# Kernel tuning notes

Hardware: AMD Instinct MI355X
Metric: run time of the kernel (lower is better)

The kernel has to match this reference:

```python
import jax, jax.numpy as jnp
import numpy as np

C = 256
HEADS = 8
HEAD_DIM = C // HEADS
SCALE = HEAD_DIM ** -0.5
POOL = 2
LN_EPS = 1e-5


def setup_inputs() -> dict:
    key = jax.random.key(0)
    ks = jax.random.split(key, 10)
    B, H, W = 8, 64, 64
    std = 0.02
    return {
        "x": jax.random.normal(ks[0], (B, C, H, W), jnp.float32),
        "Wq": jax.random.normal(ks[1], (HEADS, C), jnp.float32) * std,
        "Wk": jax.random.normal(ks[2], (HEADS, C), jnp.float32) * std,
        "Wv": jax.random.normal(ks[3], (C, C), jnp.float32) * std,
        "Wsr": jax.random.normal(ks[4], (C, C), jnp.float32) * (2.0 / C) ** 0.5,
        "bsr": jnp.zeros((C,), jnp.float32),
        "gamma": jnp.ones((C,), jnp.float32),
        "beta": jnp.zeros((C,), jnp.float32),
        "Wp": jax.random.normal(ks[5], (C, C), jnp.float32) * std,
        "bp": jnp.zeros((C,), jnp.float32),
    }


def reference(x, Wq, Wk, Wv, Wsr, bsr, gamma, beta, Wp, bp):
    B, Cc, H, W = x.shape
    N = H * W
    # tokens [B, N, C]
    tok = x.reshape(B, Cc, N).transpose(0, 2, 1)
    # q: Linear(C -> heads), per-head scalar query  [B, heads, N]
    q = jnp.einsum("bnc,hc->bhn", tok, Wq)
    # spatial reduction: avgpool(pool_ratio) then 1x1 conv
    xp = x.reshape(B, Cc, H // POOL, POOL, W // POOL, POOL).mean(axis=(3, 5))
    xs = jnp.einsum("bchw,oc->bohw", xp, Wsr) + bsr[None, :, None, None]
    M = (H // POOL) * (W // POOL)
    x_ = xs.reshape(B, Cc, M).transpose(0, 2, 1)  # [B, M, C]
    # LayerNorm + GELU (exact erf, torch default)
    mu = x_.mean(-1, keepdims=True)
    var = ((x_ - mu) ** 2).mean(-1, keepdims=True)
    x_ = (x_ - mu) * jax.lax.rsqrt(var + LN_EPS) * gamma + beta
    x_ = jax.nn.gelu(x_, approximate=False)
    # k: per-head scalar key [B, heads, M]; v: [B, heads, M, head_dim]
    k = jnp.einsum("bmc,hc->bhm", x_, Wk)
    v = jnp.einsum("bmc,oc->bmo", x_, Wv).reshape(B, M, HEADS, HEAD_DIM).transpose(0, 2, 1, 3)
    # rank-1 attention scores [B, heads, N, M]
    attn = jax.nn.softmax(q[:, :, :, None] * k[:, :, None, :] * SCALE, axis=-1)
    out = jnp.einsum("bhnm,bhmd->bhnd", attn, v)  # [B, heads, N, head_dim]
    out = out.transpose(0, 2, 1, 3).reshape(B, N, Cc)
    out = out @ Wp.T + bp
    return out.transpose(0, 2, 1).reshape(B, Cc, H, W)
```

## Files before the change

kernel.cpp:

```cpp
#include <hip/hip_runtime.h>
#include <math.h>


#define NH 8
#define NJ 8
#define NT (NH * NJ)
#define SCALE 0.17677669529663687f

__device__ __constant__ float INVFACT[NJ] = {
    1.0f, 1.0f, 0.5f, 1.6666666666666666e-01f, 4.1666666666666664e-02f,
    8.3333333333333332e-03f, 1.3888888888888889e-03f, 1.9841269841269841e-04f};

__global__ void k0_q_prep(const float* __restrict__ x, const float* __restrict__ Wq,
                          const float* __restrict__ Wsr, const float* __restrict__ Wv,
                          float* __restrict__ q01, float* __restrict__ WsrT,
                          float* __restrict__ WvT) {
    __shared__ float wq[NH * 128];
    const int tid = threadIdx.x;
    const int blk = blockIdx.x;
    if (blk < 256) {
        const int b = blk >> 5, half = (blk >> 4) & 1, nt = blk & 15;
#pragma unroll
        for (int r = 0; r < 4; ++r) {
            int idx = r * 256 + tid;
            int h = idx >> 7, cc = idx & 127;
            wq[idx] = Wq[h * 256 + half * 128 + cc];
        }
        __syncthreads();
        const int n = nt * 256 + tid;
        const float* xb = x + (((size_t)b << 8) + half * 128) * 4096 + n;
        float acc[NH] = {};
#pragma unroll 8
        for (int c = 0; c < 128; ++c) {
            float xv = xb[(size_t)c << 12];
#pragma unroll
            for (int h = 0; h < NH; ++h) acc[h] += xv * wq[h * 128 + c];
        }
#pragma unroll
        for (int h = 0; h < NH; ++h)
            q01[((size_t)(half * 64 + b * 8 + h) << 12) + n] = acc[h];
    } else {
        const float* W = (blk < 288) ? Wsr : Wv;
        float* WT = (blk < 288) ? WsrT : WvT;
        const int c0 = (blk & 31) * 8;
#pragma unroll
        for (int r = 0; r < 2; ++r) {
            int fidx = r * 256 + tid;
            int c = c0 + (fidx >> 6), o4 = (fidx & 63) * 4;
            float4 t;
            t.x = W[(size_t)(o4 + 0) * 256 + c];
            t.y = W[(size_t)(o4 + 1) * 256 + c];
            t.z = W[(size_t)(o4 + 2) * 256 + c];
            t.w = W[(size_t)(o4 + 3) * 256 + c];
            *(float4*)&WT[(size_t)c * 256 + o4] = t;
        }
    }
}

__global__ void ka_mega(const float* __restrict__ x, const float* __restrict__ WsrT,
                        const float* __restrict__ bsr, const float* __restrict__ WvT,
                        const float* __restrict__ gamma, const float* __restrict__ beta,
                        const float* __restrict__ Wk,
                        float* __restrict__ v, float* __restrict__ kout) {
    __shared__ float smem[20352];
    float* a_pool = smem;
    float* wpan   = smem + 1152;
    float* g_lds  = smem + 9472;
    float4* wkv   = (float4*)(smem + 17792);
    float4* glv   = (float4*)(smem + 19840);
    float4* blv   = (float4*)(smem + 20096);

    const int tid = threadIdx.x;
    const int blk = blockIdx.x;
    const int b = blk >> 5, mt = blk & 31;
    const int m0 = mt * 32;
    const int i2 = mt;

    const int ccs = tid >> 3, jg = tid & 7;
    const int mg = tid & 7, og = tid >> 3;

    const float4* Wk4 = (const float4*)Wk;
    wkv[tid] = Wk4[tid];
    wkv[256 + tid] = Wk4[256 + tid];
    if (tid < 64) {
        glv[tid] = ((const float4*)gamma)[tid];
        blv[tid] = ((const float4*)beta)[tid];
    }

    float acc[4][8] = {};
    for (int c0 = 0; c0 < 256; c0 += 32) {
        __syncthreads();
        {
            const float* p = x + ((size_t)(b * 256 + c0 + ccs) << 12) +
                             i2 * 128 + jg * 8;
            float4 r00 = *(const float4*)p;
            float4 r01 = *(const float4*)(p + 4);
            float4 r10 = *(const float4*)(p + 64);
            float4 r11 = *(const float4*)(p + 68);
            float4 pv;
            pv.x = 0.25f * ((r00.x + r00.y) + (r10.x + r10.y));
            pv.y = 0.25f * ((r00.z + r00.w) + (r10.z + r10.w));
            pv.z = 0.25f * ((r01.x + r01.y) + (r11.x + r11.y));
            pv.w = 0.25f * ((r01.z + r01.w) + (r11.z + r11.w));
            *(float4*)&a_pool[ccs * 36 + jg * 4] = pv;
        }
#pragma unroll
        for (int r = 0; r < 8; ++r) {
            int fidx = r * 256 + tid;
            int cc = fidx >> 6, o4 = (fidx & 63) * 4;
            *(float4*)&wpan[cc * 260 + o4] =
                *(const float4*)&WsrT[(size_t)(c0 + cc) * 256 + o4];
        }
        __syncthreads();
#pragma unroll
        for (int cc = 0; cc < 32; ++cc) {
            float4 av = *(const float4*)&a_pool[cc * 36 + mg * 4];
            float4 b0 = *(const float4*)&wpan[cc * 260 + og * 8];
            float4 b1 = *(const float4*)&wpan[cc * 260 + og * 8 + 4];
            float am[4] = {av.x, av.y, av.z, av.w};
            float bo[8] = {b0.x, b0.y, b0.z, b0.w, b1.x, b1.y, b1.z, b1.w};
#pragma unroll
            for (int i = 0; i < 4; ++i)
#pragma unroll
                for (int j = 0; j < 8; ++j) acc[i][j] += am[i] * bo[j];
        }
    }
    {
        float4 bs0 = *(const float4*)&bsr[og * 8];
        float4 bs1 = *(const float4*)&bsr[og * 8 + 4];
#pragma unroll
        for (int i = 0; i < 4; ++i) {
            float4 w0, w1;
            w0.x = acc[i][0] + bs0.x; w0.y = acc[i][1] + bs0.y;
            w0.z = acc[i][2] + bs0.z; w0.w = acc[i][3] + bs0.w;
            w1.x = acc[i][4] + bs1.x; w1.y = acc[i][5] + bs1.y;
            w1.z = acc[i][6] + bs1.z; w1.w = acc[i][7] + bs1.w;
            *(float4*)&g_lds[(mg * 4 + i) * 260 + og * 8] = w0;
            *(float4*)&g_lds[(mg * 4 + i) * 260 + og * 8 + 4] = w1;
        }
    }
    __syncthreads();

    const int wave = tid >> 6, lane = tid & 63;
    const float4 g4 = glv[lane], be4 = blv[lane];
#pragma unroll
    for (int ti = 0; ti < 8; ++ti) {
        const int mm = wave * 8 + ti;
        float4 vv = *(const float4*)&g_lds[mm * 260 + lane * 4];
        float s = (vv.x + vv.y) + (vv.z + vv.w);
        float s2 = (vv.x * vv.x + vv.y * vv.y) + (vv.z * vv.z + vv.w * vv.w);
#pragma unroll
        for (int off = 1; off < 64; off <<= 1) {
            s += __shfl_xor(s, off);
            s2 += __shfl_xor(s2, off);
        }
        const float mu = s * (1.f / 256.f);
        const float rstd = rsqrtf(s2 * (1.f / 256.f) - mu * mu + 1e-5f);
        float4 gg;
        {
            float xh;
            xh = (vv.x - mu) * rstd * g4.x + be4.x;
            gg.x = 0.5f * xh * (1.f + erff(xh * 0.70710678118654752f));
            xh = (vv.y - mu) * rstd * g4.y + be4.y;
            gg.y = 0.5f * xh * (1.f + erff(xh * 0.70710678118654752f));
            xh = (vv.z - mu) * rstd * g4.z + be4.z;
            gg.z = 0.5f * xh * (1.f + erff(xh * 0.70710678118654752f));
            xh = (vv.w - mu) * rstd * g4.w + be4.w;
            gg.w = 0.5f * xh * (1.f + erff(xh * 0.70710678118654752f));
        }
        *(float4*)&g_lds[mm * 260 + lane * 4] = gg;
        float acck[NH];
#pragma unroll
        for (int h = 0; h < NH; ++h) {
            float4 w = wkv[h * 64 + lane];
            acck[h] = (gg.x * w.x + gg.y * w.y) + (gg.z * w.z + gg.w * w.w);
        }
#pragma unroll
        for (int off = 1; off < 64; off <<= 1)
#pragma unroll
            for (int h = 0; h < NH; ++h) acck[h] += __shfl_xor(acck[h], off);
        if (lane == 0) {
#pragma unroll
            for (int h = 0; h < NH; ++h)
                kout[((size_t)(b * 8 + h) << 10) + m0 + mm] = acck[h];
        }
    }

    float accv[4][8] = {};
    for (int c0 = 0; c0 < 256; c0 += 32) {
        __syncthreads();
#pragma unroll
        for (int r = 0; r < 8; ++r) {
            int fidx = r * 256 + tid;
            int cc = fidx >> 6, o4 = (fidx & 63) * 4;
            *(float4*)&wpan[cc * 260 + o4] =
                *(const float4*)&WvT[(size_t)(c0 + cc) * 256 + o4];
        }
        __syncthreads();
#pragma unroll
        for (int cc = 0; cc < 32; ++cc) {
            const int c = c0 + cc;
            float a0 = g_lds[(mg * 4 + 0) * 260 + c];
            float a1 = g_lds[(mg * 4 + 1) * 260 + c];
            float a2 = g_lds[(mg * 4 + 2) * 260 + c];
            float a3 = g_lds[(mg * 4 + 3) * 260 + c];
            float4 b0 = *(const float4*)&wpan[cc * 260 + og * 8];
            float4 b1 = *(const float4*)&wpan[cc * 260 + og * 8 + 4];
            float bo[8] = {b0.x, b0.y, b0.z, b0.w, b1.x, b1.y, b1.z, b1.w};
#pragma unroll
            for (int j = 0; j < 8; ++j) {
                accv[0][j] += a0 * bo[j];
                accv[1][j] += a1 * bo[j];
                accv[2][j] += a2 * bo[j];
                accv[3][j] += a3 * bo[j];
            }
        }
    }
#pragma unroll
    for (int i = 0; i < 4; ++i) {
        float4 r0, r1;
        r0.x = accv[i][0]; r0.y = accv[i][1]; r0.z = accv[i][2]; r0.w = accv[i][3];
        r1.x = accv[i][4]; r1.y = accv[i][5]; r1.z = accv[i][6]; r1.w = accv[i][7];
        float* dst = &v[((size_t)(b << 10) + m0 + mg * 4 + i) * 256 + og * 8];
        *(float4*)dst = r0;
        *(float4*)(dst + 4) = r1;
    }
}

__global__ void kc_moments_project(const float* __restrict__ kin,
                                   const float* __restrict__ v,
                                   const float* __restrict__ Wp,
                                   float* __restrict__ P, float* __restrict__ S2) {
    const int bh = blockIdx.x;
    const int h = bh & 7, b = bh >> 3;
    const int tid = threadIdx.x;
    const int g = tid >> 5, d = tid & 31;
    float accM[NJ] = {};
    float accS[NJ] = {};
    const float* kb = kin + ((size_t)bh << 10);
    const float* vb = v + ((size_t)b << 18) + h * 32 + d;
#pragma unroll 4
    for (int mi = 0; mi < 128; ++mi) {
        int m = g * 128 + mi;
        float km = kb[m];
        float w = vb[(size_t)m << 8];
        float t = w, ts = 1.f;
#pragma unroll
        for (int j = 0; j < NJ; ++j) {
            accM[j] += t;
            accS[j] += ts;
            t *= km;
            ts *= km;
        }
    }
    __shared__ float red[8][NJ][33];
#pragma unroll
    for (int j = 0; j < NJ; ++j) red[g][j][d] = accM[j];
    if (d == 0) {
#pragma unroll
        for (int j = 0; j < NJ; ++j) red[g][j][32] = accS[j];
    }
    __syncthreads();
    __shared__ float Ms[NJ][33];
    for (int idx = tid; idx < NJ * 33; idx += 256) {
        int j = idx / 33, dd = idx % 33;
        float sum = 0.f;
#pragma unroll
        for (int gg = 0; gg < 8; ++gg) sum += red[gg][j][dd];
        Ms[j][dd] = sum * INVFACT[j];
    }
    __syncthreads();
    const int c = tid;
    float wp[32];
    const float* wrow = Wp + c * 256 + h * 32;
#pragma unroll
    for (int i = 0; i < 8; ++i) {
        float4 t = *(const float4*)(wrow + i * 4);
        wp[i * 4 + 0] = t.x; wp[i * 4 + 1] = t.y;
        wp[i * 4 + 2] = t.z; wp[i * 4 + 3] = t.w;
    }
#pragma unroll
    for (int j = 0; j < NJ; ++j) {
        float s = 0.f;
#pragma unroll
        for (int dd = 0; dd < 32; ++dd) s += wp[dd] * Ms[j][dd];
        P[((size_t)bh * NJ + j) * 256 + c] = s;
    }
    if (tid < NJ) S2[bh * NJ + tid] = Ms[tid][32];
}

__global__ void kd_out(const float* __restrict__ q01, const float* __restrict__ S2,
                       const float* __restrict__ P, const float* __restrict__ bp,
                       float* __restrict__ out) {
    __shared__ float p_lds[NT * 264];
    __shared__ float coef_lds[NT * 32];
    __shared__ float s2l[NT];
    const int tid = threadIdx.x;
    const int b = blockIdx.x >> 7, nt = blockIdx.x & 127;
    const int n0 = nt * 32;
    if (tid < NT) s2l[tid] = S2[b * NT + tid];
    const float* Pb = P + (size_t)b * (NT * 256);
#pragma unroll
    for (int r = 0; r < 16; ++r) {
        int fidx = r * 256 + tid;
        int t = fidx >> 6, c4 = (fidx & 63) * 4;
        *(float4*)&p_lds[t * 264 + c4] = *(const float4*)&Pb[t * 256 + c4];
    }
    __syncthreads();
    {
        const int n = tid & 31, h = tid >> 5;
        size_t qi = ((size_t)(b * NH + h) << 12) + n0 + n;
        float a = (q01[qi] + q01[qi + ((size_t)64 << 12)]) * SCALE;
        float den = s2l[h * NJ + NJ - 1];
#pragma unroll
        for (int j = NJ - 2; j >= 0; --j) den = den * a + s2l[h * NJ + j];
        float p = 1.0f / den;
#pragma unroll
        for (int j = 0; j < NJ; ++j) {
            coef_lds[(h * NJ + j) * 32 + n] = p;
            p *= a;
        }
    }
    __syncthreads();
    const int ng = tid & 7, og = tid >> 3;
    float acc[8][4] = {};
#pragma unroll 8
    for (int t = 0; t < NT; ++t) {
        float4 nv = *(const float4*)&coef_lds[t * 32 + ng * 4];
        float4 cv0 = *(const float4*)&p_lds[t * 264 + og * 8];
        float4 cv1 = *(const float4*)&p_lds[t * 264 + og * 8 + 4];
        float nm[4] = {nv.x, nv.y, nv.z, nv.w};
        float cm[8] = {cv0.x, cv0.y, cv0.z, cv0.w, cv1.x, cv1.y, cv1.z, cv1.w};
#pragma unroll
        for (int i = 0; i < 8; ++i)
#pragma unroll
            for (int j = 0; j < 4; ++j) acc[i][j] += cm[i] * nm[j];
    }
    float* ob = out + ((size_t)(b << 8) + og * 8) * 4096 + n0 + ng * 4;
#pragma unroll
    for (int i = 0; i < 8; ++i) {
        float bpc = bp[og * 8 + i];
        float4 r;
        r.x = acc[i][0] + bpc; r.y = acc[i][1] + bpc;
        r.z = acc[i][2] + bpc; r.w = acc[i][3] + bpc;
        *(float4*)(ob + (size_t)i * 4096) = r;
    }
}

extern "C" void kernel_launch(void* const* d_in, const int* in_sizes, int n_in,
                              void* d_out, int out_size, void* d_ws, size_t ws_size,
                              hipStream_t stream) {
    const float* x     = (const float*)d_in[0];
    const float* Wq    = (const float*)d_in[1];
    const float* Wk    = (const float*)d_in[2];
    const float* Wv    = (const float*)d_in[3];
    const float* Wsr   = (const float*)d_in[4];
    const float* bsr   = (const float*)d_in[5];
    const float* gamma = (const float*)d_in[6];
    const float* beta  = (const float*)d_in[7];
    const float* Wp    = (const float*)d_in[8];
    const float* bp    = (const float*)d_in[9];
    float* out = (float*)d_out;

    float* ws   = (float*)d_ws;
    float* vbuf = ws;
    float* q01  = vbuf + 2097152;
    float* kbuf = q01 + 524288;
    float* P    = kbuf + 65536;
    float* S2   = P + 131072;
    float* WsrT = S2 + 512;
    float* WvT  = WsrT + 65536;

    k0_q_prep<<<320, 256, 0, stream>>>(x, Wq, Wsr, Wv, q01, WsrT, WvT);
    ka_mega<<<256, 256, 0, stream>>>(x, WsrT, bsr, WvT, gamma, beta, Wk,
                                     vbuf, kbuf);
    kc_moments_project<<<64, 256, 0, stream>>>(kbuf, vbuf, Wp, P, S2);
    kd_out<<<1024, 256, 0, stream>>>(q01, S2, P, bp, out);
}
```

Baseline: 207.7 us.

## Split fused pool/SR/LN/V mega-kernel into separate higher-parallelism kernels

Replaces the single 256-block fused kernel (pool, SR GEMM, LayerNorm+GELU+k, V GEMM) with a pooling stage folded into the prep kernel, a 512-block SR GEMM, a LayerNorm/k kernel, and a 512-block V GEMM. The aim is more blocks and better occupancy for the two GEMMs, which were limited to 256 large blocks with heavy LDS use. In exchange, the intermediate pooled and normalized activations go through global memory, which adds round trips and extra kernel launches.

Measured after the change: 249.8 us. 1.2x slower.

```diff
diff --git a/kernel.cpp b/kernel.cpp
--- a/kernel.cpp
+++ b/kernel.cpp
@@ -13,8 +13,8 @@
 
 __global__ void k0_q_prep(const float* __restrict__ x, const float* __restrict__ Wq,
                           const float* __restrict__ Wsr, const float* __restrict__ Wv,
-                          float* __restrict__ q01, float* __restrict__ WsrT,
-                          float* __restrict__ WvT) {
+                          float* __restrict__ q01, float* __restrict__ xp,
+                          float* __restrict__ WsrT, float* __restrict__ WvT) {
     __shared__ float wq[NH * 128];
     const int tid = threadIdx.x;
     const int blk = blockIdx.x;
@@ -39,9 +39,20 @@
 #pragma unroll
         for (int h = 0; h < NH; ++h)
             q01[((size_t)(half * 64 + b * 8 + h) << 12) + n] = acc[h];
+    } else if (blk < 512) {
+        const int base = (blk - 256) * 8192;
+#pragma unroll 8
+        for (int r = 0; r < 32; ++r) {
+            int o = base + r * 256 + tid;
+            int j = o & 31, i = (o >> 5) & 31, bc = o >> 10;
+            const float* p = x + ((size_t)bc << 12) + (i * 2) * 64 + j * 2;
+            float2 t0 = *(const float2*)p;
+            float2 t1 = *(const float2*)(p + 64);
+            xp[o] = 0.25f * ((t0.x + t0.y) + (t1.x + t1.y));
+        }
     } else {
-        const float* W = (blk < 288) ? Wsr : Wv;
-        float* WT = (blk < 288) ? WsrT : WvT;
+        const float* W = (blk < 544) ? Wsr : Wv;
+        float* WT = (blk < 544) ? WsrT : WvT;
         const int c0 = (blk & 31) * 8;
 #pragma unroll
         for (int r = 0; r < 2; ++r) {
@@ -57,28 +68,52 @@
     }
 }
 
-__global__ void ka_mega(const float* __restrict__ x, const float* __restrict__ WsrT,
-                        const float* __restrict__ bsr, const float* __restrict__ WvT,
-                        const float* __restrict__ gamma, const float* __restrict__ beta,
-                        const float* __restrict__ Wk,
-                        float* __restrict__ v, float* __restrict__ kout) {
-    __shared__ float smem[20352];
-    float* a_pool = smem;
-    float* wpan   = smem + 1152;
-    float* g_lds  = smem + 9472;
-    float4* wkv   = (float4*)(smem + 17792);
-    float4* glv   = (float4*)(smem + 19840);
-    float4* blv   = (float4*)(smem + 20096);
-
-    const int tid = threadIdx.x;
-    const int blk = blockIdx.x;
-    const int b = blk >> 5, mt = blk & 31;
-    const int m0 = mt * 32;
-    const int i2 = mt;
-
-    const int ccs = tid >> 3, jg = tid & 7;
-    const int mg = tid & 7, og = tid >> 3;
-
+__global__ void ka_sr(const float* __restrict__ xp, const float* __restrict__ WsrT,
+                      const float* __restrict__ bsr, float* __restrict__ xt) {
+    __shared__ float bsl[256 * 68];
+    const int tid = threadIdx.x;
+    const int ot = blockIdx.x;
+    const int mt = blockIdx.y;
+    const int b  = blockIdx.z;
+    const int o0 = ot * 64, m0 = mt * 64;
+#pragma unroll
+    for (int r = 0; r < 16; ++r) {
+        int fidx = r * 256 + tid;
+        int c = fidx >> 4, o4 = (fidx & 15) * 4;
+        *(float4*)&bsl[c * 68 + o4] = *(const float4*)&WsrT[(size_t)c * 256 + o0 + o4];
+    }
+    __syncthreads();
+    const int mg = tid & 15, og = tid >> 4;
+    const float* ap = xp + ((size_t)b << 18) + m0 + mg * 4;
+    float acc[4][4] = {};
+#pragma unroll 8
+    for (int c = 0; c < 256; ++c) {
+        float4 av = *(const float4*)(ap + ((size_t)c << 10));
+        float4 bv = *(const float4*)&bsl[c * 68 + og * 4];
+        float am[4] = {av.x, av.y, av.z, av.w};
+        float bo[4] = {bv.x, bv.y, bv.z, bv.w};
+#pragma unroll
+        for (int i = 0; i < 4; ++i)
+#pragma unroll
+            for (int j = 0; j < 4; ++j) acc[i][j] += am[i] * bo[j];
+    }
+    float4 bias = *(const float4*)&bsr[o0 + og * 4];
+#pragma unroll
+    for (int i = 0; i < 4; ++i) {
+        float4 r;
+        r.x = acc[i][0] + bias.x; r.y = acc[i][1] + bias.y;
+        r.z = acc[i][2] + bias.z; r.w = acc[i][3] + bias.w;
+        *(float4*)&xt[((size_t)(b << 10) + m0 + mg * 4 + i) * 256 + o0 + og * 4] = r;
+    }
+}
+
+__global__ void kb_ln(float* __restrict__ xt, const float* __restrict__ gamma,
+                      const float* __restrict__ beta, const float* __restrict__ Wk,
+                      float* __restrict__ kout) {
+    __shared__ float4 wkv[NH * 64];
+    __shared__ float4 glv[64];
+    __shared__ float4 blv[64];
+    const int tid = threadIdx.x;
     const float4* Wk4 = (const float4*)Wk;
     wkv[tid] = Wk4[tid];
     wkv[256 + tid] = Wk4[256 + tid];
@@ -86,69 +121,18 @@
         glv[tid] = ((const float4*)gamma)[tid];
         blv[tid] = ((const float4*)beta)[tid];
     }
-
-    float acc[4][8] = {};
-    for (int c0 = 0; c0 < 256; c0 += 32) {
-        __syncthreads();
-        {
-            const float* p = x + ((size_t)(b * 256 + c0 + ccs) << 12) +
-                             i2 * 128 + jg * 8;
-            float4 r00 = *(const float4*)p;
-            float4 r01 = *(const float4*)(p + 4);
-            float4 r10 = *(const float4*)(p + 64);
-            float4 r11 = *(const float4*)(p + 68);
-            float4 pv;
-            pv.x = 0.25f * ((r00.x + r00.y) + (r10.x + r10.y));
-            pv.y = 0.25f * ((r00.z + r00.w) + (r10.z + r10.w));
-            pv.z = 0.25f * ((r01.x + r01.y) + (r11.x + r11.y));
-            pv.w = 0.25f * ((r01.z + r01.w) + (r11.z + r11.w));
-            *(float4*)&a_pool[ccs * 36 + jg * 4] = pv;
-        }
-#pragma unroll
-        for (int r = 0; r < 8; ++r) {
-            int fidx = r * 256 + tid;
-            int cc = fidx >> 6, o4 = (fidx & 63) * 4;
-            *(float4*)&wpan[cc * 260 + o4] =
-                *(const float4*)&WsrT[(size_t)(c0 + cc) * 256 + o4];
-        }
-        __syncthreads();
-#pragma unroll
-        for (int cc = 0; cc < 32; ++cc) {
-            float4 av = *(const float4*)&a_pool[cc * 36 + mg * 4];
-            float4 b0 = *(const float4*)&wpan[cc * 260 + og * 8];
-            float4 b1 = *(const float4*)&wpan[cc * 260 + og * 8 + 4];
-            float am[4] = {av.x, av.y, av.z, av.w};
-            float bo[8] = {b0.x, b0.y, b0.z, b0.w, b1.x, b1.y, b1.z, b1.w};
-#pragma unroll
-            for (int i = 0; i < 4; ++i)
-#pragma unroll
-                for (int j = 0; j < 8; ++j) acc[i][j] += am[i] * bo[j];
-        }
-    }
-    {
-        float4 bs0 = *(const float4*)&bsr[og * 8];
-        float4 bs1 = *(const float4*)&bsr[og * 8 + 4];
-#pragma unroll
-        for (int i = 0; i < 4; ++i) {
-            float4 w0, w1;
-            w0.x = acc[i][0] + bs0.x; w0.y = acc[i][1] + bs0.y;
-            w0.z = acc[i][2] + bs0.z; w0.w = acc[i][3] + bs0.w;
-            w1.x = acc[i][4] + bs1.x; w1.y = acc[i][5] + bs1.y;
-            w1.z = acc[i][6] + bs1.z; w1.w = acc[i][7] + bs1.w;
-            *(float4*)&g_lds[(mg * 4 + i) * 260 + og * 8] = w0;
-            *(float4*)&g_lds[(mg * 4 + i) * 260 + og * 8 + 4] = w1;
-        }
-    }
-    __syncthreads();
-
+    __syncthreads();
     const int wave = tid >> 6, lane = tid & 63;
+    const int b = blockIdx.x >> 5;
+    const int mb = blockIdx.x & 31;
     const float4 g4 = glv[lane], be4 = blv[lane];
-#pragma unroll
+#pragma unroll 2
     for (int ti = 0; ti < 8; ++ti) {
-        const int mm = wave * 8 + ti;
-        float4 vv = *(const float4*)&g_lds[mm * 260 + lane * 4];
-        float s = (vv.x + vv.y) + (vv.z + vv.w);
-        float s2 = (vv.x * vv.x + vv.y * vv.y) + (vv.z * vv.z + vv.w * vv.w);
+        const int m = mb * 32 + wave * 8 + ti;
+        float4* row = (float4*)(xt + ((size_t)(b << 10) + m) * 256);
+        float4 v = row[lane];
+        float s = (v.x + v.y) + (v.z + v.w);
+        float s2 = (v.x * v.x + v.y * v.y) + (v.z * v.z + v.w * v.w);
 #pragma unroll
         for (int off = 1; off < 64; off <<= 1) {
             s += __shfl_xor(s, off);
@@ -156,74 +140,82 @@
         }
         const float mu = s * (1.f / 256.f);
         const float rstd = rsqrtf(s2 * (1.f / 256.f) - mu * mu + 1e-5f);
-        float4 gg;
+        float4 g;
         {
             float xh;
-            xh = (vv.x - mu) * rstd * g4.x + be4.x;
-            gg.x = 0.5f * xh * (1.f + erff(xh * 0.70710678118654752f));
-            xh = (vv.y - mu) * rstd * g4.y + be4.y;
-            gg.y = 0.5f * xh * (1.f + erff(xh * 0.70710678118654752f));
-            xh = (vv.z - mu) * rstd * g4.z + be4.z;
-            gg.z = 0.5f * xh * (1.f + erff(xh * 0.70710678118654752f));
-            xh = (vv.w - mu) * rstd * g4.w + be4.w;
-            gg.w = 0.5f * xh * (1.f + erff(xh * 0.70710678118654752f));
-        }
-        *(float4*)&g_lds[mm * 260 + lane * 4] = gg;
-        float acck[NH];
+            xh = (v.x - mu) * rstd * g4.x + be4.x;
+            g.x = 0.5f * xh * (1.f + erff(xh * 0.70710678118654752f));
+            xh = (v.y - mu) * rstd * g4.y + be4.y;
+            g.y = 0.5f * xh * (1.f + erff(xh * 0.70710678118654752f));
+            xh = (v.z - mu) * rstd * g4.z + be4.z;
+            g.z = 0.5f * xh * (1.f + erff(xh * 0.70710678118654752f));
+            xh = (v.w - mu) * rstd * g4.w + be4.w;
+            g.w = 0.5f * xh * (1.f + erff(xh * 0.70710678118654752f));
+        }
+        row[lane] = g;
+        float acc[NH];
 #pragma unroll
         for (int h = 0; h < NH; ++h) {
             float4 w = wkv[h * 64 + lane];
-            acck[h] = (gg.x * w.x + gg.y * w.y) + (gg.z * w.z + gg.w * w.w);
-        }
-#pragma unroll
-        for (int off = 1; off < 64; off <<= 1)
-#pragma unroll
-            for (int h = 0; h < NH; ++h) acck[h] += __shfl_xor(acck[h], off);
+            acc[h] = (g.x * w.x + g.y * w.y) + (g.z * w.z + g.w * w.w);
+        }
+#pragma unroll
+        for (int off = 1; off < 64; off <<= 1) {
+#pragma unroll
+            for (int h = 0; h < NH; ++h) acc[h] += __shfl_xor(acc[h], off);
+        }
         if (lane == 0) {
 #pragma unroll
             for (int h = 0; h < NH; ++h)
-                kout[((size_t)(b * 8 + h) << 10) + m0 + mm] = acck[h];
-        }
-    }
-
-    float accv[4][8] = {};
-    for (int c0 = 0; c0 < 256; c0 += 32) {
-        __syncthreads();
-#pragma unroll
-        for (int r = 0; r < 8; ++r) {
-            int fidx = r * 256 + tid;
-            int cc = fidx >> 6, o4 = (fidx & 63) * 4;
-            *(float4*)&wpan[cc * 260 + o4] =
-                *(const float4*)&WvT[(size_t)(c0 + cc) * 256 + o4];
-        }
-        __syncthreads();
-#pragma unroll
-        for (int cc = 0; cc < 32; ++cc) {
-            const int c = c0 + cc;
-            float a0 = g_lds[(mg * 4 + 0) * 260 + c];
-            float a1 = g_lds[(mg * 4 + 1) * 260 + c];
-            float a2 = g_lds[(mg * 4 + 2) * 260 + c];
-            float a3 = g_lds[(mg * 4 + 3) * 260 + c];
-            float4 b0 = *(const float4*)&wpan[cc * 260 + og * 8];
-            float4 b1 = *(const float4*)&wpan[cc * 260 + og * 8 + 4];
-            float bo[8] = {b0.x, b0.y, b0.z, b0.w, b1.x, b1.y, b1.z, b1.w};
-#pragma unroll
-            for (int j = 0; j < 8; ++j) {
-                accv[0][j] += a0 * bo[j];
-                accv[1][j] += a1 * bo[j];
-                accv[2][j] += a2 * bo[j];
-                accv[3][j] += a3 * bo[j];
-            }
-        }
+                kout[((size_t)(b * NH + h) << 10) + m] = acc[h];
+        }
+    }
+}
+
+__global__ void kc_v(const float* __restrict__ g, const float* __restrict__ WvT,
+                     float* __restrict__ v) {
+    __shared__ float bsl[256 * 68];
+    const int tid = threadIdx.x;
+    const int ot = blockIdx.x;
+    const int mt = blockIdx.y;
+    const int b  = blockIdx.z;
+    const int o0 = ot * 64, m0 = mt * 64;
+#pragma unroll
+    for (int r = 0; r < 16; ++r) {
+        int fidx = r * 256 + tid;
+        int c = fidx >> 4, o4 = (fidx & 15) * 4;
+        *(float4*)&bsl[c * 68 + o4] = *(const float4*)&WvT[(size_t)c * 256 + o0 + o4];
+    }
+    __syncthreads();
+    const int mg = tid & 15, og = tid >> 4;
+    const float* ap = g + ((size_t)b << 18) + (size_t)(m0 + mg * 4) * 256;
+    float acc[4][4] = {};
+#pragma unroll 4
+    for (int c4 = 0; c4 < 64; ++c4) {
+        float4 a0 = *(const float4*)(ap + c4 * 4);
+        float4 a1 = *(const float4*)(ap + 256 + c4 * 4);
+        float4 a2 = *(const float4*)(ap + 512 + c4 * 4);
+        float4 a3 = *(const float4*)(ap + 768 + c4 * 4);
+        float4 b0 = *(const float4*)&bsl[(c4 * 4 + 0) * 68 + og * 4];
+        float4 b1 = *(const float4*)&bsl[(c4 * 4 + 1) * 68 + og * 4];
+        float4 b2 = *(const float4*)&bsl[(c4 * 4 + 2) * 68 + og * 4];
+        float4 b3 = *(const float4*)&bsl[(c4 * 4 + 3) * 68 + og * 4];
+        float av[4][4] = {{a0.x, a0.y, a0.z, a0.w}, {a1.x, a1.y, a1.z, a1.w},
+                          {a2.x, a2.y, a2.z, a2.w}, {a3.x, a3.y, a3.z, a3.w}};
+        float bv[4][4] = {{b0.x, b0.y, b0.z, b0.w}, {b1.x, b1.y, b1.z, b1.w},
+                          {b2.x, b2.y, b2.z, b2.w}, {b3.x, b3.y, b3.z, b3.w}};
+#pragma unroll
+        for (int i = 0; i < 4; ++i)
+#pragma unroll
+            for (int k = 0; k < 4; ++k)
+#pragma unroll
+                for (int j = 0; j < 4; ++j) acc[i][j] += av[i][k] * bv[k][j];
     }
 #pragma unroll
     for (int i = 0; i < 4; ++i) {
-        float4 r0, r1;
-        r0.x = accv[i][0]; r0.y = accv[i][1]; r0.z = accv[i][2]; r0.w = accv[i][3];
-        r1.x = accv[i][4]; r1.y = accv[i][5]; r1.z = accv[i][6]; r1.w = accv[i][7];
-        float* dst = &v[((size_t)(b << 10) + m0 + mg * 4 + i) * 256 + og * 8];
-        *(float4*)dst = r0;
-        *(float4*)(dst + 4) = r1;
+        float4 r;
+        r.x = acc[i][0]; r.y = acc[i][1]; r.z = acc[i][2]; r.w = acc[i][3];
+        *(float4*)&v[((size_t)(b << 10) + m0 + mg * 4 + i) * 256 + o0 + og * 4] = r;
     }
 }
 
@@ -363,7 +355,9 @@
     float* out = (float*)d_out;
 
     float* ws   = (float*)d_ws;
-    float* vbuf = ws;
+    float* xp   = ws;
+    float* xt   = xp + 2097152;
+    float* vbuf = xt + 2097152;
     float* q01  = vbuf + 2097152;
     float* kbuf = q01 + 524288;
     float* P    = kbuf + 65536;
@@ -371,9 +365,10 @@
     float* WsrT = S2 + 512;
     float* WvT  = WsrT + 65536;
 
-    k0_q_prep<<<320, 256, 0, stream>>>(x, Wq, Wsr, Wv, q01, WsrT, WvT);
-    ka_mega<<<256, 256, 0, stream>>>(x, WsrT, bsr, WvT, gamma, beta, Wk,
-                                     vbuf, kbuf);
+    k0_q_prep<<<576, 256, 0, stream>>>(x, Wq, Wsr, Wv, q01, xp, WsrT, WvT);
+    ka_sr<<<dim3(4, 16, 8), 256, 0, stream>>>(xp, WsrT, bsr, xt);
+    kb_ln<<<256, 256, 0, stream>>>(xt, gamma, beta, Wk, kbuf);
+    kc_v<<<dim3(4, 16, 8), 256, 0, stream>>>(xt, WvT, vbuf);
     kc_moments_project<<<64, 256, 0, stream>>>(kbuf, vbuf, Wp, P, S2);
     kd_out<<<1024, 256, 0, stream>>>(q01, S2, P, bp, out);
 }
```
